# Kernel tuning notes

Hardware: AMD Instinct MI355X
Metric: run time of the kernel (lower is better)

Reference implementation:

```python
import jax, jax.numpy as jnp
import numpy as np

H = 4096
NH = 32
HD = 128
FF = 14336
EPS = 1e-6


def _rmsnorm(x, w):
    xf = x.astype(jnp.float32)
    var = jnp.mean(xf * xf, axis=-1, keepdims=True)
    return (w * (xf * jax.lax.rsqrt(var + EPS))).astype(x.dtype)


def setup_inputs() -> dict:
    key = jax.random.key(0)
    ks = jax.random.split(key, 16)
    S = 2048
    def lin(k, fan_in, shape):
        bound = 1.0 / np.sqrt(fan_in)
        return jax.random.uniform(k, shape, jnp.float32, -bound, bound)
    return {
        "hidden_states": jax.random.normal(ks[0], (S, H), jnp.float32),
        "position_ids": jnp.arange(S, dtype=jnp.int64),
        "wq": lin(ks[1], H, (NH * HD, H)), "bq": lin(ks[2], H, (NH * HD,)),
        "wk": lin(ks[3], H, (NH * HD, H)), "bk": lin(ks[4], H, (NH * HD,)),
        "wv": lin(ks[5], H, (NH * HD, H)), "bv": lin(ks[6], H, (NH * HD,)),
        "wo": lin(ks[7], H, (H, H)), "bo": lin(ks[8], H, (H,)),
        "w_gate": lin(ks[9], H, (FF, H)),
        "w_up": lin(ks[10], H, (FF, H)),
        "w_down": lin(ks[11], FF, (H, FF)),
        "ln1_w": jnp.ones((H,), jnp.float32),
        "ln2_w": jnp.ones((H,), jnp.float32),
    }


def reference(hidden_states, position_ids, wq, bq, wk, bk, wv, bv, wo, bo,
              w_gate, w_up, w_down, ln1_w, ln2_w):
    S = hidden_states.shape[0]
    # --- attention block ---
    x = _rmsnorm(hidden_states, ln1_w)
    q = (x @ wq.T + bq).reshape(S, NH, HD)
    k = (x @ wk.T + bk).reshape(S, NH, HD)
    v = (x @ wv.T + bv).reshape(S, NH, HD)
    scale = 1.0 / np.sqrt(HD)
    scores = jnp.einsum('qhd,khd->hqk', q.astype(jnp.float32),
                        k.astype(jnp.float32)) * scale
    causal = jnp.tril(jnp.ones((S, S), bool))  # decoder causal mask
    scores = jnp.where(causal[None, :, :], scores, -jnp.inf)
    probs = jax.nn.softmax(scores, axis=-1)
    h = jnp.einsum('hqk,khd->qhd', probs, v.astype(jnp.float32))
    attn_out = h.reshape(S, NH * HD).astype(hidden_states.dtype) @ wo.T + bo
    h1 = hidden_states + attn_out
    # --- SwiGLU MLP block ---
    y = _rmsnorm(h1, ln2_w)
    mlp = (jax.nn.silu(y @ w_gate.T) * (y @ w_up.T)) @ w_down.T
    return h1 + mlp
```

## Files before the change

kernel.cpp:

```cpp
#include <hip/hip_runtime.h>
#include <math.h>

#define H_DIM 4096
#define NHEAD 32
#define HD 128
#define FF_DIM 14336

typedef unsigned short u16;
typedef __attribute__((ext_vector_type(8))) short bf16x8;
typedef __attribute__((ext_vector_type(4))) float f32x4;
typedef __attribute__((ext_vector_type(4))) unsigned short u16x4;

typedef const __attribute__((address_space(1))) void* gas_ptr;
typedef __attribute__((address_space(3))) void* las_ptr;

__device__ __forceinline__ void gload_lds16(const void* g, void* l) {
  __builtin_amdgcn_global_load_lds((gas_ptr)g, (las_ptr)l, 16, 0, 0);
}

__device__ __forceinline__ u16 f32_to_bf16(float f) {
  unsigned int u = __float_as_uint(f);
  u = (u + 0x7FFFu + ((u >> 16) & 1u)) >> 16;
  return (u16)u;
}
__device__ __forceinline__ float bf16_to_f32(u16 x) {
  return __uint_as_float(((unsigned int)x) << 16);
}

__device__ __forceinline__ void conv4(const float* __restrict__ in,
                                      u16* __restrict__ out, long i) {
  const f32x4* p = reinterpret_cast<const f32x4*>(in) + i;
  f32x4 v = __builtin_nontemporal_load(p);
  u16x4 o;
  o.x = f32_to_bf16(v.x); o.y = f32_to_bf16(v.y);
  o.z = f32_to_bf16(v.z); o.w = f32_to_bf16(v.w);
  reinterpret_cast<u16x4*>(out)[i] = o;
}

__global__ void f2b_kernel(const float* __restrict__ in, u16* __restrict__ out, long n4) {
  long i = (long)blockIdx.x * blockDim.x + threadIdx.x;
  long stride = (long)gridDim.x * blockDim.x;
  for (; i < n4; i += stride) conv4(in, out, i);
}

__global__ void f2b3_kernel(const float* __restrict__ a, const float* __restrict__ b,
                            const float* __restrict__ c, u16* __restrict__ out, long n4each) {
  long i = (long)blockIdx.x * blockDim.x + threadIdx.x;
  long st = (long)gridDim.x * blockDim.x;
  long tot = 3 * n4each;
  for (; i < tot; i += st) {
    const float* src; long j;
    if (i < n4each)            { src = a; j = i; }
    else if (i < 2 * n4each)   { src = b; j = i - n4each; }
    else                       { src = c; j = i - 2 * n4each; }
    const f32x4* p = reinterpret_cast<const f32x4*>(src) + j;
    f32x4 v = __builtin_nontemporal_load(p);
    u16x4 o;
    o.x = f32_to_bf16(v.x); o.y = f32_to_bf16(v.y);
    o.z = f32_to_bf16(v.z); o.w = f32_to_bf16(v.w);
    reinterpret_cast<u16x4*>(out)[i] = o;
  }
}

__global__ void bias_concat_kernel(const float* __restrict__ a, const float* __restrict__ b,
                                   const float* __restrict__ c, float* __restrict__ out) {
  int i = blockIdx.x * blockDim.x + threadIdx.x;
  float v;
  if (i < 4096) v = a[i];
  else if (i < 8192) v = b[i - 4096];
  else v = c[i - 8192];
  out[i] = v;
}

__global__ void rmsnorm_kernel(const float* __restrict__ in, const float* __restrict__ w,
                               u16* __restrict__ out) {
  int row = blockIdx.x;
  int tid = threadIdx.x;
  const float4* x4 = reinterpret_cast<const float4*>(in + (size_t)row * H_DIM);
  float4 vv[4];
  float ss = 0.f;
#pragma unroll
  for (int it = 0; it < 4; ++it) {
    float4 v = x4[tid + it * 256];
    vv[it] = v;
    ss += v.x * v.x + v.y * v.y + v.z * v.z + v.w * v.w;
  }
#pragma unroll
  for (int off = 1; off < 64; off <<= 1) ss += __shfl_xor(ss, off);
  __shared__ float part[4];
  if ((tid & 63) == 0) part[tid >> 6] = ss;
  __syncthreads();
  float tot = part[0] + part[1] + part[2] + part[3];
  float rinv = rsqrtf(tot * (1.0f / H_DIM) + 1e-6f);
  const float4* w4 = reinterpret_cast<const float4*>(w);
  u16* orow = out + (size_t)row * H_DIM;
#pragma unroll
  for (int it = 0; it < 4; ++it) {
    float4 v = vv[it];
    float4 wv = w4[tid + it * 256];
    ushort4 o;
    o.x = f32_to_bf16(v.x * rinv * wv.x);
    o.y = f32_to_bf16(v.y * rinv * wv.y);
    o.z = f32_to_bf16(v.z * rinv * wv.z);
    o.w = f32_to_bf16(v.w * rinv * wv.w);
    reinterpret_cast<ushort4*>(orow)[tid + it * 256] = o;
  }
}

enum { EPI_QKV = 0, EPI_O = 1, EPI_SILU = 2, EPI_MUL = 3, EPI_PART = 4 };

template <int EPI, bool SPLIT>
__global__ __launch_bounds__(512, 2) void gemm256(
    const u16* __restrict__ A, const u16* __restrict__ B, void* __restrict__ outp,
    const float* __restrict__ bias, const void* __restrict__ extra,
    int M, int N, int K, int kLen) {
  __shared__ __align__(16) u16 As[2][256 * 64];
  __shared__ __align__(16) u16 Bs[2][256 * 64];
  const int tid = threadIdx.x;
  const int wid = tid >> 6, lane = tid & 63;
  const int lg = lane >> 4, li = lane & 15;
  const int wr = (wid >> 2) << 7;
  const int wc = (wid & 3) << 6;

  const int nbm = M >> 8, nbn = N >> 8;
  const int nb = nbm * nbn;
  int wg = (blockIdx.x & 7) * (gridDim.x >> 3) + (blockIdx.x >> 3);
  int s = 0;
  if (SPLIT) { s = wg / nb; wg -= s * nb; }
  const int m0 = (wg % nbm) << 8, n0 = (wg / nbm) << 8;
  const int kB = SPLIT ? s * kLen : 0;
  const int NT = kLen >> 6;

  const int r8 = tid >> 3;
  const int sl = ((tid & 7) ^ (r8 & 7)) << 3;
  const u16* sA[2][2];
  const u16* sB[2][2];
  int ldo[2][2];
#pragma unroll
  for (int P = 0; P < 2; ++P)
#pragma unroll
    for (int h = 0; h < 2; ++h) {
      int lr = P * 128 + h * 64 + r8;
      int ra = (lr & 63) | ((lr >> 1) & 64) | ((lr << 1) & 128);
      int rb = (lr & 31) | ((lr & 96) << 1) | ((lr & 128) >> 2);
      sA[P][h] = A + (size_t)(m0 + ra) * K + kB + sl;
      sB[P][h] = B + (size_t)(n0 + rb) * K + kB + sl;
      ldo[P][h] = (P * 128 + h * 64 + (wid << 3)) << 6;
    }

  auto stageA = [&](int P, int d, int ko) {
#pragma unroll
    for (int h = 0; h < 2; ++h)
      gload_lds16(sA[P][h] + ko, (void*)(&As[d][ldo[P][h]]));
  };
  auto stageB = [&](int P, int d, int ko) {
#pragma unroll
    for (int h = 0; h < 2; ++h)
      gload_lds16(sB[P][h] + ko, (void*)(&Bs[d][ldo[P][h]]));
  };

  bf16x8 a[4][2], b[4][2];
  f32x4 acc[8][4] = {};
  const int s20 = (lg ^ (li & 7)) << 3;
  const int s21 = ((4 + lg) ^ (li & 7)) << 3;

  auto ldA = [&](int d, int set) {
#pragma unroll
    for (int i = 0; i < 4; ++i) {
      int g = wr + set * 64 + i * 16;
      int lb = (g & 63) | ((g >> 1) & 64) | ((g << 1) & 128);
      const u16* base = &As[d][(lb + li) << 6];
      a[i][0] = *reinterpret_cast<const bf16x8*>(base + s20);
      a[i][1] = *reinterpret_cast<const bf16x8*>(base + s21);
    }
  };
  auto ldB = [&](int d, int set) {
#pragma unroll
    for (int jj = 0; jj < 2; ++jj) {
      int hh = wc + (set * 2 + jj) * 16;
      int lb = ((hh & 32) << 2) | ((hh & 192) >> 1) | (hh & 31);
      const u16* base = &Bs[d][(lb + li) << 6];
      b[set * 2 + jj][0] = *reinterpret_cast<const bf16x8*>(base + s20);
      b[set * 2 + jj][1] = *reinterpret_cast<const bf16x8*>(base + s21);
    }
  };
  auto mm = [&](int iset, int jset) {
    __builtin_amdgcn_s_setprio(1);
#pragma unroll
    for (int i = 0; i < 4; ++i)
#pragma unroll
      for (int jj = 0; jj < 2; ++jj)
#pragma unroll
        for (int kk = 0; kk < 2; ++kk)
          acc[iset * 4 + i][jset * 2 + jj] = __builtin_amdgcn_mfma_f32_16x16x32_bf16(
              a[i][kk], b[jset * 2 + jj][kk], acc[iset * 4 + i][jset * 2 + jj], 0, 0, 0);
    __builtin_amdgcn_s_setprio(0);
  };

  stageA(0, 0, 0); stageB(0, 0, 0); stageB(1, 0, 0); stageA(1, 0, 0);
  if (NT > 1) {
    stageA(0, 1, 64); stageB(0, 1, 64); stageB(1, 1, 64); stageA(1, 1, 64);
    asm volatile("s_waitcnt vmcnt(8)" ::: "memory");
  } else {
    asm volatile("s_waitcnt vmcnt(0)" ::: "memory");
  }
  __builtin_amdgcn_s_barrier();

  for (int t = 0; t < NT; ++t) {
    int d = t & 1;
    bool pf = (t + 2) < NT;
    int ko = (t + 2) << 6;
    ldB(d, 0); ldA(d, 0);
    __builtin_amdgcn_s_barrier();
    mm(0, 0);
    __builtin_amdgcn_s_barrier();
    ldB(d, 1);
    if (pf) { stageA(0, d, ko); stageB(0, d, ko); }
    __builtin_amdgcn_s_barrier();
    mm(0, 1);
    __builtin_amdgcn_s_barrier();
    ldA(d, 1);
    if (pf) stageB(1, d, ko);
    __builtin_amdgcn_s_barrier();
    mm(1, 0);
    __builtin_amdgcn_s_barrier();
    if (pf) {
      stageA(1, d, ko);
      asm volatile("s_waitcnt vmcnt(6)" ::: "memory");
    } else {
      asm volatile("s_waitcnt vmcnt(0)" ::: "memory");
    }
    __builtin_amdgcn_s_barrier();
    mm(1, 1);
    __builtin_amdgcn_s_barrier();
  }

#pragma unroll
  for (int i = 0; i < 8; ++i) {
#pragma unroll
    for (int j = 0; j < 4; ++j) {
      int col = n0 + wc + j * 16 + li;
      float bv = 0.f;
      if (EPI == EPI_QKV || EPI == EPI_O) bv = bias[col];
      if (EPI == EPI_PART && bias != nullptr && s == 0) bv = bias[col];
#pragma unroll
      for (int r = 0; r < 4; ++r) {
        int row = m0 + wr + i * 16 + lg * 4 + r;
        float v = acc[i][j][r] + bv;
        size_t idx = (size_t)row * N + col;
        if (EPI == EPI_QKV) {
          ((u16*)outp)[idx] = f32_to_bf16(v);
        } else if (EPI == EPI_O) {
          const float* res = (const float*)extra;
          ((float*)outp)[idx] = res[idx] + v;
        } else if (EPI == EPI_SILU) {
          float sv = v / (1.f + __expf(-v));
          ((u16*)outp)[idx] = f32_to_bf16(sv);
        } else if (EPI == EPI_MUL) {
          const u16* sg = (const u16*)extra;
          ((u16*)outp)[idx] = f32_to_bf16(v * bf16_to_f32(sg[idx]));
        } else {
          ((float*)outp)[(size_t)s * M * N + idx] = v;
        }
      }
    }
  }
}

__global__ void reduce_down(const float* __restrict__ p, const float* __restrict__ res,
                            float* __restrict__ out, long n4, long str4) {
  long i = (long)blockIdx.x * blockDim.x + threadIdx.x;
  long st = (long)gridDim.x * blockDim.x;
  for (; i < n4; i += st) {
    f32x4 h = reinterpret_cast<const f32x4*>(res)[i];
    f32x4 p0 = __builtin_nontemporal_load(reinterpret_cast<const f32x4*>(p) + i);
    f32x4 p1 = __builtin_nontemporal_load(reinterpret_cast<const f32x4*>(p) + i + str4);
    f32x4 o;
    o.x = h.x + p0.x + p1.x; o.y = h.y + p0.y + p1.y;
    o.z = h.z + p0.z + p1.z; o.w = h.w + p0.w + p1.w;
    __builtin_nontemporal_store(o, reinterpret_cast<f32x4*>(out) + i);
  }
}

__global__ void transpose_kernel(const u16* __restrict__ in, u16* __restrict__ out,
                                 int S, int ldin) {
  __shared__ __align__(16) u16 t[64][80];
  int sbT = S >> 6;
  int bs = blockIdx.x % sbT, bc = blockIdx.x / sbT;
  int s0 = bs << 6, c0 = bc << 6;
  int tid = threadIdx.x;
  int ir = tid >> 3;
  int jc = (tid & 7) * 8;
#pragma unroll
  for (int h = 0; h < 2; ++h) {
    int sr = ir + h * 32;
    uint4 v = *reinterpret_cast<const uint4*>(in + (size_t)(s0 + sr) * ldin + c0 + jc);
    *reinterpret_cast<uint4*>(&t[sr][jc]) = v;
  }
  __syncthreads();
  int d = tid >> 3;
  int ss = (tid & 7) * 8;
#pragma unroll
  for (int h = 0; h < 2; ++h) {
    int dd = d + h * 32;
    u16 tmp[8];
#pragma unroll
    for (int e = 0; e < 8; ++e) tmp[e] = t[ss + e][dd];
    *reinterpret_cast<uint4*>(out + (size_t)(c0 + dd) * S + s0 + ss) =
        *reinterpret_cast<const uint4*>(tmp);
  }
}

__global__ __launch_bounds__(256) void attn_kernel(
    const u16* __restrict__ q, const u16* __restrict__ k,
    const u16* __restrict__ vt, u16* __restrict__ o, int S, int ldqk) {
  __shared__ __align__(16) u16 plds[4][16 * 64];
  int tid = threadIdx.x, wid = tid >> 6, lane = tid & 63;
  int lg = lane >> 4, li = lane & 15;
  int nwg = gridDim.x;
  int sbid = (blockIdx.x & 7) * (nwg >> 3) + (blockIdx.x >> 3);
  int task = sbid * 4 + wid;
  int pairs = S >> 5;
  int head = task / pairs;
  int pi = task - head * pairs;
  const float scale = 0.08838834764831845f;
  u16* pl = plds[wid];
  int ntiles = S >> 4;

  for (int tix = 0; tix < 2; ++tix) {
    int qt = tix ? (ntiles - 1 - pi) : pi;
    int q0 = qt << 4;

    bf16x8 aq[4];
    {
      const u16* qrow = q + (size_t)(q0 + li) * ldqk + head * HD + lg * 8;
#pragma unroll
      for (int ks = 0; ks < 4; ++ks)
        aq[ks] = *reinterpret_cast<const bf16x8*>(qrow + ks * 32);
    }

    f32x4 oacc[8] = {};
    float m_run[4], l_run[4];
#pragma unroll
    for (int r = 0; r < 4; ++r) { m_run[r] = -INFINITY; l_run[r] = 0.f; }

    int nkb = ((q0 + 15) >> 6) + 1;
    for (int kb = 0; kb < nkb; ++kb) {
      int kvbase = kb << 6;
      f32x4 sacc[4] = {};
#pragma unroll
      for (int cf = 0; cf < 4; ++cf) {
        const u16* krow = k + (size_t)(kvbase + cf * 16 + li) * ldqk + head * HD + lg * 8;
#pragma unroll
        for (int ks = 0; ks < 4; ++ks) {
          bf16x8 bk = *reinterpret_cast<const bf16x8*>(krow + ks * 32);
          sacc[cf] = __builtin_amdgcn_mfma_f32_16x16x32_bf16(aq[ks], bk, sacc[cf], 0, 0, 0);
        }
      }
      bool bnd = (kvbase + 63) > q0;
      float alpha[4];
#pragma unroll
      for (int r = 0; r < 4; ++r) {
        int row = q0 + lg * 4 + r;
#pragma unroll
        for (int cf = 0; cf < 4; ++cf) {
          float sv = sacc[cf][r] * scale;
          if (bnd && (kvbase + cf * 16 + li) > row) sv = -INFINITY;
          sacc[cf][r] = sv;
        }
        float mv = fmaxf(fmaxf(sacc[0][r], sacc[1][r]),
                         fmaxf(sacc[2][r], sacc[3][r]));
#pragma unroll
        for (int off = 1; off < 16; off <<= 1) mv = fmaxf(mv, __shfl_xor(mv, off));
        float mnew = fmaxf(m_run[r], mv);
        alpha[r] = __expf(m_run[r] - mnew);
        m_run[r] = mnew;
        float ps = 0.f;
#pragma unroll
        for (int cf = 0; cf < 4; ++cf) {
          float pv = __expf(sacc[cf][r] - mnew);
          sacc[cf][r] = pv;
          ps += pv;
        }
#pragma unroll
        for (int off = 1; off < 16; off <<= 1) ps += __shfl_xor(ps, off);
        l_run[r] = l_run[r] * alpha[r] + ps;
      }
#pragma unroll
      for (int df = 0; df < 8; ++df)
#pragma unroll
        for (int r = 0; r < 4; ++r) oacc[df][r] *= alpha[r];
#pragma unroll
      for (int cf = 0; cf < 4; ++cf)
#pragma unroll
        for (int r = 0; r < 4; ++r) {
          int row = lg * 4 + r;
          int el = row * 64 + cf * 16 + li;
          pl[el ^ ((row & 7) << 3)] = f32_to_bf16(sacc[cf][r]);
        }
      asm volatile("s_waitcnt lgkmcnt(0)" ::: "memory");
      __builtin_amdgcn_sched_barrier(0);
#pragma unroll
      for (int kk = 0; kk < 2; ++kk) {
        int el = li * 64 + kk * 32 + lg * 8;
        bf16x8 pa = *reinterpret_cast<const bf16x8*>(pl + (el ^ ((li & 7) << 3)));
        const u16* vb = vt + kvbase + kk * 32 + lg * 8;
#pragma unroll
        for (int df = 0; df < 8; ++df) {
          bf16x8 bv = *reinterpret_cast<const bf16x8*>(vb + (size_t)(head * HD + df * 16 + li) * S);
          oacc[df] = __builtin_amdgcn_mfma_f32_16x16x32_bf16(pa, bv, oacc[df], 0, 0, 0);
        }
      }
    }
#pragma unroll
    for (int r = 0; r < 4; ++r) {
      float inv = 1.0f / l_run[r];
      int row = q0 + lg * 4 + r;
      u16* orow = o + (size_t)row * H_DIM + head * HD;
#pragma unroll
      for (int df = 0; df < 8; ++df)
        orow[df * 16 + li] = f32_to_bf16(oacc[df][r] * inv);
    }
  }
}

extern "C" void kernel_launch(void* const* d_in, const int* in_sizes, int n_in,
                              void* d_out, int out_size, void* d_ws, size_t ws_size,
                              hipStream_t stream) {
  (void)n_in; (void)out_size;
  const float* hidden = (const float*)d_in[0];
  const float* wq = (const float*)d_in[2];
  const float* bq = (const float*)d_in[3];
  const float* wk = (const float*)d_in[4];
  const float* bk = (const float*)d_in[5];
  const float* wv = (const float*)d_in[6];
  const float* bv = (const float*)d_in[7];
  const float* wo = (const float*)d_in[8];
  const float* bo = (const float*)d_in[9];
  const float* wg = (const float*)d_in[10];
  const float* wu = (const float*)d_in[11];
  const float* wd = (const float*)d_in[12];
  const float* ln1 = (const float*)d_in[13];
  const float* ln2 = (const float*)d_in[14];
  float* out = (float*)d_out;

  int S = in_sizes[0] / H_DIM;
  int NQKV = 3 * H_DIM;

  char* ws = (char*)d_ws;
  size_t off = 0;
  auto alloc = [&](size_t bytes) {
    void* p = ws + off;
    off += (bytes + 255) & ~(size_t)255;
    return p;
  };
  u16* wbuf = (u16*)alloc((size_t)FF_DIM * H_DIM * 2);
  u16* xb   = (u16*)alloc((size_t)S * H_DIM * 2);
  u16* qkv  = (u16*)alloc((size_t)S * NQKV * 2);
  u16* vtb  = (u16*)alloc((size_t)S * H_DIM * 2);
  u16* hat  = (u16*)alloc((size_t)S * H_DIM * 2);
  float* h1 = (float*)alloc((size_t)S * H_DIM * 4);
  u16* sg   = (u16*)alloc((size_t)S * FF_DIM * 2);
  u16* tb   = (u16*)alloc((size_t)S * FF_DIM * 2);
  float* bcat = (float*)alloc((size_t)NQKV * 4);
  if (off > ws_size) return;
  float* pbuf = (float*)qkv;

  dim3 b256(256), b512(512);
  long nHH4 = (long)H_DIM * H_DIM / 4;
  long nFH4 = (long)FF_DIM * H_DIM / 4;
  int gQKV3 = (S / 256) * (NQKV / 256);
  int gO    = 2 * (S / 256) * (H_DIM / 256);
  int gFF   = (S / 256) * (FF_DIM / 256);
  int gDW   = 2 * (S / 256) * (H_DIM / 256);
  long n4HH = (long)S * H_DIM / 4;
  int gAttn = (NHEAD * (S / 16)) / 2 / 4;

  rmsnorm_kernel<<<S, b256, 0, stream>>>(hidden, ln1, xb);
  bias_concat_kernel<<<NQKV / 256, b256, 0, stream>>>(bq, bk, bv, bcat);
  f2b3_kernel<<<4096, b256, 0, stream>>>(wq, wk, wv, wbuf, nHH4);
  gemm256<EPI_QKV, false><<<gQKV3, b512, 0, stream>>>(xb, wbuf, qkv, bcat, nullptr,
                                                      S, NQKV, H_DIM, H_DIM);
  transpose_kernel<<<(S / 64) * (H_DIM / 64), b256, 0, stream>>>(qkv + 2 * H_DIM, vtb, S, NQKV);
  attn_kernel<<<gAttn, b256, 0, stream>>>(qkv, qkv + H_DIM, vtb, hat, S, NQKV);
  f2b_kernel<<<4096, b256, 0, stream>>>(wo, wbuf, nHH4);
  gemm256<EPI_PART, true><<<gO, b512, 0, stream>>>(hat, wbuf, pbuf, bo, nullptr,
                                                   S, H_DIM, H_DIM, H_DIM / 2);
  reduce_down<<<2048, b256, 0, stream>>>(pbuf, hidden, h1, n4HH, n4HH);

  rmsnorm_kernel<<<S, b256, 0, stream>>>(h1, ln2, xb);
  f2b_kernel<<<4096, b256, 0, stream>>>(wg, wbuf, nFH4);
  gemm256<EPI_SILU, false><<<gFF, b512, 0, stream>>>(xb, wbuf, sg, nullptr, nullptr,
                                                     S, FF_DIM, H_DIM, H_DIM);
  f2b_kernel<<<4096, b256, 0, stream>>>(wu, wbuf, nFH4);
  gemm256<EPI_MUL, false><<<gFF, b512, 0, stream>>>(xb, wbuf, tb, nullptr, sg,
                                                    S, FF_DIM, H_DIM, H_DIM);
  f2b_kernel<<<4096, b256, 0, stream>>>(wd, wbuf, nFH4);
  gemm256<EPI_PART, true><<<gDW, b512, 0, stream>>>(tb, wbuf, pbuf, nullptr, nullptr,
                                                    S, H_DIM, FF_DIM, FF_DIM / 2);
  reduce_down<<<2048, b256, 0, stream>>>(pbuf, h1, out, n4HH, n4HH);
}
```

Baseline: 1.481 ms.

## Fuse gate and up projections into one GEMM with SwiGLU epilogue

Merges the separate gate and up GEMMs into a single kernel. Each 256-row B tile holds 128 gate rows and 128 up rows, so one block produces a 256x128 output tile and applies silu(g)*u in registers. This removes the bf16 sg intermediate write/read and one GEMM launch, and shares each A tile across both projections. The cost is a second bf16 weight buffer in the workspace and a changed B-tile row mapping for the GLU path.

Result: no change. 1.495 ms (median of 3 runs) (+0.9%).

```diff
diff --git a/kernel.cpp b/kernel.cpp
--- a/kernel.cpp
+++ b/kernel.cpp
@@ -107,12 +107,12 @@
   }
 }
 
-enum { EPI_QKV = 0, EPI_O = 1, EPI_SILU = 2, EPI_MUL = 3, EPI_PART = 4 };
+enum { EPI_QKV = 0, EPI_O = 1, EPI_SILU = 2, EPI_MUL = 3, EPI_PART = 4, EPI_GLU = 5 };
 
 template <int EPI, bool SPLIT>
 __global__ __launch_bounds__(512, 2) void gemm256(
-    const u16* __restrict__ A, const u16* __restrict__ B, void* __restrict__ outp,
-    const float* __restrict__ bias, const void* __restrict__ extra,
+    const u16* __restrict__ A, const u16* __restrict__ B, const u16* __restrict__ Bu,
+    void* __restrict__ outp, const float* __restrict__ bias, const void* __restrict__ extra,
     int M, int N, int K, int kLen) {
   __shared__ __align__(16) u16 As[2][256 * 64];
   __shared__ __align__(16) u16 Bs[2][256 * 64];
@@ -121,13 +121,16 @@
   const int lg = lane >> 4, li = lane & 15;
   const int wr = (wid >> 2) << 7;
   const int wc = (wid & 3) << 6;
-
-  const int nbm = M >> 8, nbn = N >> 8;
+  const int wcg = (wid & 3) << 5;
+
+  const int nbm = M >> 8;
+  const int nbn = (EPI == EPI_GLU) ? (N >> 7) : (N >> 8);
   const int nb = nbm * nbn;
   int wg = (blockIdx.x & 7) * (gridDim.x >> 3) + (blockIdx.x >> 3);
   int s = 0;
   if (SPLIT) { s = wg / nb; wg -= s * nb; }
-  const int m0 = (wg % nbm) << 8, n0 = (wg / nbm) << 8;
+  const int m0 = (wg % nbm) << 8;
+  const int n0 = (EPI == EPI_GLU) ? ((wg / nbm) << 7) : ((wg / nbm) << 8);
   const int kB = SPLIT ? s * kLen : 0;
   const int NT = kLen >> 6;
 
@@ -142,9 +145,14 @@
     for (int h = 0; h < 2; ++h) {
       int lr = P * 128 + h * 64 + r8;
       int ra = (lr & 63) | ((lr >> 1) & 64) | ((lr << 1) & 128);
-      int rb = (lr & 31) | ((lr & 96) << 1) | ((lr & 128) >> 2);
       sA[P][h] = A + (size_t)(m0 + ra) * K + kB + sl;
-      sB[P][h] = B + (size_t)(n0 + rb) * K + kB + sl;
+      if (EPI == EPI_GLU) {
+        const u16* srcm = P ? Bu : B;
+        sB[P][h] = srcm + (size_t)(n0 + h * 64 + r8) * K + sl;
+      } else {
+        int rb = (lr & 31) | ((lr & 96) << 1) | ((lr & 128) >> 2);
+        sB[P][h] = B + (size_t)(n0 + rb) * K + kB + sl;
+      }
       ldo[P][h] = (P * 128 + h * 64 + (wid << 3)) << 6;
     }
 
@@ -177,8 +185,13 @@
   auto ldB = [&](int d, int set) {
 #pragma unroll
     for (int jj = 0; jj < 2; ++jj) {
-      int hh = wc + (set * 2 + jj) * 16;
-      int lb = ((hh & 32) << 2) | ((hh & 192) >> 1) | (hh & 31);
+      int lb;
+      if (EPI == EPI_GLU) {
+        lb = set * 128 + wcg + jj * 16;
+      } else {
+        int hh = wc + (set * 2 + jj) * 16;
+        lb = ((hh & 32) << 2) | ((hh & 192) >> 1) | (hh & 31);
+      }
       const u16* base = &Bs[d][(lb + li) << 6];
       b[set * 2 + jj][0] = *reinterpret_cast<const bf16x8*>(base + s20);
       b[set * 2 + jj][1] = *reinterpret_cast<const bf16x8*>(base + s21);
@@ -235,6 +248,24 @@
     __builtin_amdgcn_s_barrier();
   }
 
+  if (EPI == EPI_GLU) {
+#pragma unroll
+    for (int i = 0; i < 8; ++i) {
+#pragma unroll
+      for (int jj = 0; jj < 2; ++jj) {
+        int col = n0 + wcg + jj * 16 + li;
+#pragma unroll
+        for (int r = 0; r < 4; ++r) {
+          int row = m0 + wr + i * 16 + lg * 4 + r;
+          float g = acc[i][jj][r];
+          float u = acc[i][2 + jj][r];
+          float sv = (g / (1.f + __expf(-g))) * u;
+          ((u16*)outp)[(size_t)row * N + col] = f32_to_bf16(sv);
+        }
+      }
+    }
+    return;
+  }
 #pragma unroll
   for (int i = 0; i < 8; ++i) {
 #pragma unroll
@@ -454,13 +485,13 @@
     off += (bytes + 255) & ~(size_t)255;
     return p;
   };
-  u16* wbuf = (u16*)alloc((size_t)FF_DIM * H_DIM * 2);
+  u16* wbuf  = (u16*)alloc((size_t)FF_DIM * H_DIM * 2);
+  u16* wbufU = (u16*)alloc((size_t)FF_DIM * H_DIM * 2);
   u16* xb   = (u16*)alloc((size_t)S * H_DIM * 2);
   u16* qkv  = (u16*)alloc((size_t)S * NQKV * 2);
   u16* vtb  = (u16*)alloc((size_t)S * H_DIM * 2);
   u16* hat  = (u16*)alloc((size_t)S * H_DIM * 2);
   float* h1 = (float*)alloc((size_t)S * H_DIM * 4);
-  u16* sg   = (u16*)alloc((size_t)S * FF_DIM * 2);
   u16* tb   = (u16*)alloc((size_t)S * FF_DIM * 2);
   float* bcat = (float*)alloc((size_t)NQKV * 4);
   if (off > ws_size) return;
@@ -471,7 +502,7 @@
   long nFH4 = (long)FF_DIM * H_DIM / 4;
   int gQKV3 = (S / 256) * (NQKV / 256);
   int gO    = 2 * (S / 256) * (H_DIM / 256);
-  int gFF   = (S / 256) * (FF_DIM / 256);
+  int gGLU  = (S / 256) * (FF_DIM / 128);
   int gDW   = 2 * (S / 256) * (H_DIM / 256);
   long n4HH = (long)S * H_DIM / 4;
   int gAttn = (NHEAD * (S / 16)) / 2 / 4;
@@ -479,24 +510,22 @@
   rmsnorm_kernel<<<S, b256, 0, stream>>>(hidden, ln1, xb);
   bias_concat_kernel<<<NQKV / 256, b256, 0, stream>>>(bq, bk, bv, bcat);
   f2b3_kernel<<<4096, b256, 0, stream>>>(wq, wk, wv, wbuf, nHH4);
-  gemm256<EPI_QKV, false><<<gQKV3, b512, 0, stream>>>(xb, wbuf, qkv, bcat, nullptr,
-                                                      S, NQKV, H_DIM, H_DIM);
+  gemm256<EPI_QKV, false><<<gQKV3, b512, 0, stream>>>(
+      xb, wbuf, nullptr, qkv, bcat, nullptr, S, NQKV, H_DIM, H_DIM);
   transpose_kernel<<<(S / 64) * (H_DIM / 64), b256, 0, stream>>>(qkv + 2 * H_DIM, vtb, S, NQKV);
   attn_kernel<<<gAttn, b256, 0, stream>>>(qkv, qkv + H_DIM, vtb, hat, S, NQKV);
   f2b_kernel<<<4096, b256, 0, stream>>>(wo, wbuf, nHH4);
-  gemm256<EPI_PART, true><<<gO, b512, 0, stream>>>(hat, wbuf, pbuf, bo, nullptr,
-                                                   S, H_DIM, H_DIM, H_DIM / 2);
+  gemm256<EPI_PART, true><<<gO, b512, 0, stream>>>(
+      hat, wbuf, nullptr, pbuf, bo, nullptr, S, H_DIM, H_DIM, H_DIM / 2);
   reduce_down<<<2048, b256, 0, stream>>>(pbuf, hidden, h1, n4HH, n4HH);
 
   rmsnorm_kernel<<<S, b256, 0, stream>>>(h1, ln2, xb);
   f2b_kernel<<<4096, b256, 0, stream>>>(wg, wbuf, nFH4);
-  gemm256<EPI_SILU, false><<<gFF, b512, 0, stream>>>(xb, wbuf, sg, nullptr, nullptr,
-                                                     S, FF_DIM, H_DIM, H_DIM);
-  f2b_kernel<<<4096, b256, 0, stream>>>(wu, wbuf, nFH4);
-  gemm256<EPI_MUL, false><<<gFF, b512, 0, stream>>>(xb, wbuf, tb, nullptr, sg,
-                                                    S, FF_DIM, H_DIM, H_DIM);
+  f2b_kernel<<<4096, b256, 0, stream>>>(wu, wbufU, nFH4);
+  gemm256<EPI_GLU, false><<<gGLU, b512, 0, stream>>>(
+      xb, wbuf, wbufU, tb, nullptr, nullptr, S, FF_DIM, H_DIM, H_DIM);
   f2b_kernel<<<4096, b256, 0, stream>>>(wd, wbuf, nFH4);
-  gemm256<EPI_PART, true><<<gDW, b512, 0, stream>>>(tb, wbuf, pbuf, nullptr, nullptr,
-                                                    S, H_DIM, FF_DIM, FF_DIM / 2);
+  gemm256<EPI_PART, true><<<gDW, b512, 0, stream>>>(
+      tb, wbuf, nullptr, pbuf, nullptr, nullptr, S, H_DIM, FF_DIM, FF_DIM / 2);
   reduce_down<<<2048, b256, 0, stream>>>(pbuf, h1, out, n4HH, n4HH);
 }
```
